# Kernel tuning notes

Measured on AMD Instinct MI355X. Metric: run time of the kernel, lower is better.

Reference implementation:

```python
import jax, jax.numpy as jnp
import numpy as np

N = 50000
T = 6
E = 800000
F_IN = 64
HID = 64
HEADS = 4
NEG_SLOPE = 0.2
BN_EPS = 1e-5


def _gat_layer(x, src, dst, W, att_src, att_dst, bias, concat):
    # x: [N, Fin]; W: [Fin, H*C]; att_*: [H, C]; src/dst: [E+N] (self loops appended)
    n = x.shape[0]
    H, C = att_src.shape
    xl = (x @ W).reshape(n, H, C)                     # [N, H, C]
    a_src = jnp.sum(xl * att_src[None], axis=-1)      # [N, H]
    a_dst = jnp.sum(xl * att_dst[None], axis=-1)      # [N, H]
    e = jax.nn.leaky_relu(a_src[src] + a_dst[dst], NEG_SLOPE)  # [E', H]
    # segment softmax over destination nodes (every node has a self loop)
    m = jax.ops.segment_max(e, dst, num_segments=n)
    ex = jnp.exp(e - m[dst])
    s = jax.ops.segment_sum(ex, dst, num_segments=n)
    alpha = ex / (s[dst] + 1e-16)                     # [E', H]
    msg = alpha[:, :, None] * xl[src]                 # [E', H, C]
    out = jax.ops.segment_sum(msg, dst, num_segments=n)  # [N, H, C]
    if concat:
        out = out.reshape(n, H * C)
    else:
        out = out.mean(axis=1)
    return out + bias


def _forward(x_seq, edge_index, W1, as1, ad1, b1, W2, as2, ad2, b2,
             cw1, cb1, g1, be1, cw2, cb2, g2, be2, lw1, lb1, lw2, lb2):
    n = x_seq.shape[1]
    self_loop = jnp.arange(n, dtype=edge_index.dtype)
    src = jnp.concatenate([edge_index[0], self_loop])
    dst = jnp.concatenate([edge_index[1], self_loop])

    def per_t(x):
        h = _gat_layer(x, src, dst, W1, as1, ad1, b1, concat=True)
        h = jax.nn.elu(h)
        h = _gat_layer(h, src, dst, W2, as2, ad2, b2, concat=False)
        h = jax.nn.elu(h)
        return h                                      # [N, HID]

    temporal = jax.vmap(per_t)(x_seq)                 # [T, N, HID]
    temporal = jnp.transpose(temporal, (1, 2, 0))     # [N, HID, T]

    def conv_bn_relu(t, cw, cb, g, be):
        y = jax.lax.conv_general_dilated(
            t, cw, window_strides=(1,), padding=[(1, 1)],
            dimension_numbers=('NCH', 'OIH', 'NCH')) + cb[None, :, None]
        # BatchNorm1d in eval mode, running_mean=0, running_var=1
        y = y * (g / jnp.sqrt(1.0 + BN_EPS))[None, :, None] + be[None, :, None]
        return jax.nn.relu(y)

    t = conv_bn_relu(temporal, cw1, cb1, g1, be1)
    t = conv_bn_relu(t, cw2, cb2, g2, be2)
    pooled = t.mean(axis=-1)                          # adaptive avg pool -> [N, HID]
    h = jax.nn.relu(pooled @ lw1 + lb1)
    logits = h @ lw2 + lb2                            # [N, 1]
    return logits


def setup_inputs() -> dict:
    key = jax.random.key(0)
    ks = jax.random.split(key, 20)
    C1 = HID // HEADS  # 16
    s = 0.1
    return {
        'x_seq': jax.random.normal(ks[0], (T, N, F_IN), jnp.float32),
        'edge_index': jax.random.randint(ks[1], (2, E), 0, N, jnp.int32),
        'W1': jax.random.normal(ks[2], (F_IN, HEADS * C1), jnp.float32) * s,
        'as1': jax.random.normal(ks[3], (HEADS, C1), jnp.float32) * s,
        'ad1': jax.random.normal(ks[4], (HEADS, C1), jnp.float32) * s,
        'b1': jnp.zeros((HEADS * C1,), jnp.float32),
        'W2': jax.random.normal(ks[5], (HID, HEADS * HID), jnp.float32) * s,
        'as2': jax.random.normal(ks[6], (HEADS, HID), jnp.float32) * s,
        'ad2': jax.random.normal(ks[7], (HEADS, HID), jnp.float32) * s,
        'b2': jnp.zeros((HID,), jnp.float32),
        'cw1': jax.random.normal(ks[8], (HID, HID, 3), jnp.float32) * s,
        'cb1': jnp.zeros((HID,), jnp.float32),
        'g1': jnp.ones((HID,), jnp.float32),
        'be1': jnp.zeros((HID,), jnp.float32),
        'cw2': jax.random.normal(ks[9], (HID, HID, 3), jnp.float32) * s,
        'cb2': jnp.zeros((HID,), jnp.float32),
        'g2': jnp.ones((HID,), jnp.float32),
        'be2': jnp.zeros((HID,), jnp.float32),
        'lw1': jax.random.normal(ks[10], (HID, HID // 2), jnp.float32) * s,
        'lb1': jnp.zeros((HID // 2,), jnp.float32),
        'lw2': jax.random.normal(ks[11], (HID // 2, 1), jnp.float32) * s,
        'lb2': jnp.zeros((1,), jnp.float32),
    }


def reference(x_seq, edge_index, W1, as1, ad1, b1, W2, as2, ad2, b2,
              cw1, cb1, g1, be1, cw2, cb2, g2, be2, lw1, lb1, lw2, lb2):
    return _forward(x_seq, edge_index, W1, as1, ad1, b1, W2, as2, ad2, b2,
                    cw1, cb1, g1, be1, cw2, cb2, g2, be2, lw1, lb1, lw2, lb2)
```

## Files before the change

kernel.cpp:

```cpp
#include <hip/hip_runtime.h>
#include <math.h>

#define NN 50000
#define EE 800000
#define TT 6

__device__ __forceinline__ float lrelu(float x){ return x > 0.f ? x : 0.2f*x; }
__device__ __forceinline__ float eluf(float x){ return x > 0.f ? x : expm1f(x); }

__global__ void k_init_counts(int* __restrict__ c){
  int i = blockIdx.x*256 + threadIdx.x;
  if (i < NN) c[i] = 1;
}

__global__ void k_hist(const int* __restrict__ dst, int* __restrict__ c){
  int i = blockIdx.x*256 + threadIdx.x;
  if (i < EE) atomicAdd(&c[dst[i]], 1);
}

__global__ void k_scanA(const int* __restrict__ cnt, int* __restrict__ excl,
                        int* __restrict__ bsum){
  __shared__ int sh[1024];
  int tid = threadIdx.x;
  int i = blockIdx.x*1024 + tid;
  int v = (i < NN) ? cnt[i] : 0;
  int x = v;
  sh[tid] = x; __syncthreads();
  for (int off = 1; off < 1024; off <<= 1){
    int y = (tid >= off) ? sh[tid - off] : 0;
    __syncthreads();
    x += y; sh[tid] = x; __syncthreads();
  }
  if (i < NN) excl[i] = x - v;
  if (tid == 1023) bsum[blockIdx.x] = x;
}

__global__ void k_scanB(int* __restrict__ bsum, int nb){
  if (threadIdx.x == 0){
    int run = 0;
    for (int b = 0; b < nb; ++b){ int t = bsum[b]; bsum[b] = run; run += t; }
  }
}

__global__ void k_scanC(const int* __restrict__ excl, const int* __restrict__ bsum,
                        int* __restrict__ rowptr, int* __restrict__ cursor){
  int i = blockIdx.x*1024 + threadIdx.x;
  if (i < NN){
    int v = excl[i] + bsum[blockIdx.x];
    rowptr[i] = v; cursor[i] = v;
  }
  if (i == 0) rowptr[NN] = EE + NN;
}

__global__ void k_scatter(const int* __restrict__ ei, int* __restrict__ cursor,
                          int* __restrict__ csr){
  int i = blockIdx.x*256 + threadIdx.x;
  if (i < EE){
    int d = ei[EE + i];
    int p = atomicAdd(&cursor[d], 1);
    csr[p] = ei[i];
  } else if (i < EE + NN){
    int v = i - EE;
    int p = atomicAdd(&cursor[v], 1);
    csr[p] = v;
  }
}

__global__ void k_prep(const float* __restrict__ W1, const float* __restrict__ as1,
                       const float* __restrict__ ad1,
                       const float* __restrict__ W2, const float* __restrict__ as2,
                       const float* __restrict__ ad2,
                       const float* __restrict__ cw1, const float* __restrict__ cw2,
                       const float* __restrict__ lw1,
                       float* __restrict__ Was1, float* __restrict__ Wad1,
                       float* __restrict__ Wat2, float* __restrict__ Wb,
                       float4* __restrict__ wq1, float4* __restrict__ wq2,
                       float* __restrict__ lw1t){
  int tid = threadIdx.x;
  int k = tid >> 2, h = tid & 3;
  float s1 = 0.f, d1 = 0.f, s2 = 0.f, d2 = 0.f;
  for (int c = 0; c < 16; ++c){
    float w = W1[k*64 + h*16 + c];
    s1 += w * as1[h*16 + c];
    d1 += w * ad1[h*16 + c];
  }
  for (int c = 0; c < 64; ++c){
    float w = W2[k*256 + h*64 + c];
    s2 += w * as2[h*64 + c];
    d2 += w * ad2[h*64 + c];
  }
  Was1[k*4+h] = s1; Wad1[k*4+h] = d1;
  Wat2[k*8 + h] = s2; Wat2[k*8 + 4 + h] = d2;
  for (int idx = tid; idx < 256*64; idx += 256){
    int kf = idx >> 6, c = idx & 63;
    int hh = kf >> 6, kk = kf & 63;
    Wb[idx] = W2[kk*256 + hh*64 + c];
  }
  for (int idx = tid; idx < 64*64; idx += 256){
    int o = idx >> 6, i = idx & 63;
    wq1[idx] = make_float4(cw1[o*192+i*3], cw1[o*192+i*3+1], cw1[o*192+i*3+2], 0.f);
    wq2[idx] = make_float4(cw2[o*192+i*3], cw2[o*192+i*3+1], cw2[o*192+i*3+2], 0.f);
  }
  for (int idx = tid; idx < 32*64; idx += 256){
    int j = idx >> 6, kk = idx & 63;
    lw1t[idx] = lw1[kk*32 + j];
  }
}

__global__ __launch_bounds__(256) void k_gemm_att1(const float* __restrict__ A,
                            const float* __restrict__ W,
                            const float* __restrict__ Was, const float* __restrict__ Wad,
                            float* __restrict__ Xl, float* __restrict__ a_src,
                            float* __restrict__ a_dst){
  __shared__ float At[64][16];
  int tid = threadIdx.x;
  int r0 = blockIdx.x * 16;
  {
    const float4* A4 = (const float4*)(A + (size_t)r0*64);
    float4 v = A4[tid];
    int r = tid >> 4, k4 = (tid & 15) << 2;
    At[k4+0][r] = v.x; At[k4+1][r] = v.y;
    At[k4+2][r] = v.z; At[k4+3][r] = v.w;
  }
  __syncthreads();
  int col = tid & 63;
  int rbase = (tid >> 6) << 2;
  float acc0=0.f, acc1=0.f, acc2=0.f, acc3=0.f;
  for (int k = 0; k < 64; ++k){
    float w = W[k*64 + col];
    float4 a4 = *(const float4*)&At[k][rbase];
    acc0 += a4.x*w; acc1 += a4.y*w; acc2 += a4.z*w; acc3 += a4.w*w;
  }
  Xl[(size_t)(r0+rbase+0)*64 + col] = acc0;
  Xl[(size_t)(r0+rbase+1)*64 + col] = acc1;
  Xl[(size_t)(r0+rbase+2)*64 + col] = acc2;
  Xl[(size_t)(r0+rbase+3)*64 + col] = acc3;
  if (tid < 128){
    int r = tid >> 3, jx = tid & 7;
    int h = jx & 3;
    const float* Wv = (jx < 4) ? Was : Wad;
    float a = 0.f;
    for (int k = 0; k < 64; ++k) a += At[k][r] * Wv[k*4 + h];
    if (jx < 4) a_src[(r0 + r)*4 + h] = a;
    else        a_dst[(r0 + r)*4 + h] = a;
  }
}

__global__ __launch_bounds__(256) void k_agg1(
                       const float* __restrict__ xl, const float* __restrict__ a_src,
                       const float* __restrict__ a_dst, const float* __restrict__ b1,
                       const float* __restrict__ Wat2,
                       const int* __restrict__ rowptr, const int* __restrict__ csr,
                       float* __restrict__ h1,
                       float* __restrict__ a_src2, float* __restrict__ a_dst2){
  int lane = threadIdx.x & 63;
  int wid  = threadIdx.x >> 6;
  int n = blockIdx.x*4 + wid;
  int h = lane >> 4;
  float ad = a_dst[n*4 + h];
  int rs = rowptr[n], re = rowptr[n+1];
  float s = 0.f, acc = 0.f;
  int j = rs;
  for (; j + 4 <= re; j += 4){
    int sn0=csr[j], sn1=csr[j+1], sn2=csr[j+2], sn3=csr[j+3];
    float e0=a_src[sn0*4+h], e1=a_src[sn1*4+h], e2=a_src[sn2*4+h], e3=a_src[sn3*4+h];
    float x0=xl[(size_t)sn0*64+lane], x1=xl[(size_t)sn1*64+lane];
    float x2=xl[(size_t)sn2*64+lane], x3=xl[(size_t)sn3*64+lane];
    float p0=__expf(lrelu(e0+ad)), p1=__expf(lrelu(e1+ad));
    float p2=__expf(lrelu(e2+ad)), p3=__expf(lrelu(e3+ad));
    s += p0; acc += p0*x0;
    s += p1; acc += p1*x1;
    s += p2; acc += p2*x2;
    s += p3; acc += p3*x3;
  }
  for (; j < re; ++j){
    int sn = csr[j];
    float p = __expf(lrelu(a_src[sn*4+h] + ad));
    float x = xl[(size_t)sn*64 + lane];
    s += p; acc += p*x;
  }
  float hv = eluf(acc/(s + 1e-16f) + b1[lane]);
  h1[(size_t)n*64 + lane] = hv;
  float4 wA = ((const float4*)Wat2)[lane*2];
  float4 wB = ((const float4*)Wat2)[lane*2 + 1];
  float p[8];
  p[0]=hv*wA.x; p[1]=hv*wA.y; p[2]=hv*wA.z; p[3]=hv*wA.w;
  p[4]=hv*wB.x; p[5]=hv*wB.y; p[6]=hv*wB.z; p[7]=hv*wB.w;
#pragma unroll
  for (int off = 32; off >= 1; off >>= 1){
#pragma unroll
    for (int q = 0; q < 8; ++q) p[q] += __shfl_xor(p[q], off);
  }
  if (lane == 0){
    ((float4*)a_src2)[n] = make_float4(p[0],p[1],p[2],p[3]);
    ((float4*)a_dst2)[n] = make_float4(p[4],p[5],p[6],p[7]);
  }
}

__global__ __launch_bounds__(256) void k_agg2(
                       const float* __restrict__ h1, const float* __restrict__ a_src,
                       const float* __restrict__ a_dst,
                       const int* __restrict__ rowptr, const int* __restrict__ csr,
                       float* __restrict__ agg){
  int lane = threadIdx.x & 63;
  int wid  = threadIdx.x >> 6;
  int n = blockIdx.x*4 + wid;
  float4 ad = ((const float4*)a_dst)[n];
  int rs = rowptr[n], re = rowptr[n+1];
  float s0=0.f,s1=0.f,s2=0.f,s3=0.f;
  float g0=0.f,g1=0.f,g2=0.f,g3=0.f;
  int j = rs;
  for (; j + 4 <= re; j += 4){
    int sa=csr[j], sb=csr[j+1], sc=csr[j+2], sd=csr[j+3];
    float4 ea = ((const float4*)a_src)[sa];
    float4 eb = ((const float4*)a_src)[sb];
    float4 ec = ((const float4*)a_src)[sc];
    float4 ed = ((const float4*)a_src)[sd];
    float xa = h1[(size_t)sa*64 + lane];
    float xb = h1[(size_t)sb*64 + lane];
    float xc = h1[(size_t)sc*64 + lane];
    float xd = h1[(size_t)sd*64 + lane];
    float pa0=__expf(lrelu(ea.x+ad.x)), pa1=__expf(lrelu(ea.y+ad.y));
    float pa2=__expf(lrelu(ea.z+ad.z)), pa3=__expf(lrelu(ea.w+ad.w));
    float pb0=__expf(lrelu(eb.x+ad.x)), pb1=__expf(lrelu(eb.y+ad.y));
    float pb2=__expf(lrelu(eb.z+ad.z)), pb3=__expf(lrelu(eb.w+ad.w));
    float pc0=__expf(lrelu(ec.x+ad.x)), pc1=__expf(lrelu(ec.y+ad.y));
    float pc2=__expf(lrelu(ec.z+ad.z)), pc3=__expf(lrelu(ec.w+ad.w));
    float pd0=__expf(lrelu(ed.x+ad.x)), pd1=__expf(lrelu(ed.y+ad.y));
    float pd2=__expf(lrelu(ed.z+ad.z)), pd3=__expf(lrelu(ed.w+ad.w));
    s0 += pa0+pb0+pc0+pd0; g0 += pa0*xa + pb0*xb + pc0*xc + pd0*xd;
    s1 += pa1+pb1+pc1+pd1; g1 += pa1*xa + pb1*xb + pc1*xc + pd1*xd;
    s2 += pa2+pb2+pc2+pd2; g2 += pa2*xa + pb2*xb + pc2*xc + pd2*xd;
    s3 += pa3+pb3+pc3+pd3; g3 += pa3*xa + pb3*xb + pc3*xc + pd3*xd;
  }
  for (; j < re; ++j){
    int sn = csr[j];
    float4 ev = ((const float4*)a_src)[sn];
    float x = h1[(size_t)sn*64 + lane];
    float p0=__expf(lrelu(ev.x+ad.x)), p1=__expf(lrelu(ev.y+ad.y));
    float p2=__expf(lrelu(ev.z+ad.z)), p3=__expf(lrelu(ev.w+ad.w));
    s0 += p0; g0 += p0*x;
    s1 += p1; g1 += p1*x;
    s2 += p2; g2 += p2*x;
    s3 += p3; g3 += p3*x;
  }
  size_t base = (size_t)n*256 + lane;
  agg[base      ] = g0/(s0 + 1e-16f);
  agg[base +  64] = g1/(s1 + 1e-16f);
  agg[base + 128] = g2/(s2 + 1e-16f);
  agg[base + 192] = g3/(s3 + 1e-16f);
}

__global__ __launch_bounds__(256) void k_out2(const float* __restrict__ agg,
                                              const float* __restrict__ Wb,
                                              const float* __restrict__ b2,
                                              float* __restrict__ ht){
  __shared__ float A[64*257];
  int tid = threadIdx.x;
  int lane = tid & 63;
  int w = __builtin_amdgcn_readfirstlane(tid >> 6);
  int r0 = blockIdx.x * 64;
  for (int jj = 0; jj < 64; ++jj){
    int m = jj*256 + tid;
    int row = m >> 8, k = m & 255;
    int rsrc = r0 + row; if (rsrc >= NN) rsrc = NN-1;
    A[row*257 + k] = agg[(size_t)rsrc*256 + k];
  }
  __syncthreads();
  const float* __restrict__ Wbw = Wb + w*16;
  float acc[16];
#pragma unroll
  for (int jq = 0; jq < 16; ++jq) acc[jq] = 0.f;
  const float* Ar = A + lane*257;
#pragma unroll 8
  for (int k = 0; k < 256; ++k){
    float a = Ar[k];
#pragma unroll
    for (int jq = 0; jq < 16; ++jq) acc[jq] += a * Wbw[(k<<6) + jq];
  }
  __syncthreads();
#pragma unroll
  for (int jq = 0; jq < 16; ++jq){
    int c = w*16 + jq;
    A[lane*65 + c] = eluf(0.25f*acc[jq] + b2[c]);
  }
  __syncthreads();
  for (int jj = 0; jj < 16; ++jj){
    int m = jj*256 + tid;
    int row = m >> 6, c = m & 63;
    int rdst = r0 + row;
    if (rdst < NN) ht[(size_t)rdst*64 + c] = A[row*65 + c];
  }
}

__global__ __launch_bounds__(256) void k_conv(const float* __restrict__ htb,
    const float4* __restrict__ wq1, const float* __restrict__ cb1,
    const float* __restrict__ g1,   const float* __restrict__ be1,
    const float4* __restrict__ wq2, const float* __restrict__ cb2,
    const float* __restrict__ g2,   const float* __restrict__ be2,
    float* __restrict__ pooledG){
  __shared__ float X[64*103];
  int tid  = threadIdx.x;
  int lane = tid & 63;
  int w    = __builtin_amdgcn_readfirstlane(tid >> 6);
  int nn   = lane & 15;
  int oq   = lane >> 4;
  int n0 = blockIdx.x*16;
  int n  = n0 + nn;
  int ob = w*16 + oq*4;

#pragma unroll
  for (int k = 0; k < 4; ++k){
    int p  = k*256 + tid;
    int ch = p & 63, ns = p >> 6;
    float xv[6];
#pragma unroll
    for (int t = 0; t < 6; ++t) xv[t] = htb[((size_t)t*NN + n0 + ns)*64 + ch];
#pragma unroll
    for (int t = 0; t < 6; ++t) X[ch*103 + t*17 + ns] = xv[t];
  }
  __syncthreads();

  float acc[4][6];
#pragma unroll
  for (int q = 0; q < 4; ++q){
    float c = cb1[ob+q];
#pragma unroll
    for (int t = 0; t < 6; ++t) acc[q][t] = c;
  }
  for (int i = 0; i < 64; ++i){
    const float* xp = X + i*103 + nn;
    float x1 = xp[0], x2 = xp[17], x3 = xp[34];
    float x4 = xp[51], x5 = xp[68], x6 = xp[85];
#pragma unroll
    for (int q = 0; q < 4; ++q){
      float4 wv = wq1[(ob+q)*64 + i];
      acc[q][0] += wv.y*x1 + wv.z*x2;
      acc[q][1] += wv.x*x1 + wv.y*x2 + wv.z*x3;
      acc[q][2] += wv.x*x2 + wv.y*x3 + wv.z*x4;
      acc[q][3] += wv.x*x3 + wv.y*x4 + wv.z*x5;
      acc[q][4] += wv.x*x4 + wv.y*x5 + wv.z*x6;
      acc[q][5] += wv.x*x5 + wv.y*x6;
    }
  }
  __syncthreads();
#pragma unroll
  for (int q = 0; q < 4; ++q){
    float bns = g1[ob+q]*rsqrtf(1.f + 1e-5f), be = be1[ob+q];
    float* xp = X + (ob+q)*103 + nn;
#pragma unroll
    for (int t = 0; t < 6; ++t) xp[t*17] = fmaxf(acc[q][t]*bns + be, 0.f);
  }
  __syncthreads();

#pragma unroll
  for (int q = 0; q < 4; ++q){
    float c = cb2[ob+q];
#pragma unroll
    for (int t = 0; t < 6; ++t) acc[q][t] = c;
  }
  for (int i = 0; i < 64; ++i){
    const float* xp = X + i*103 + nn;
    float x1 = xp[0], x2 = xp[17], x3 = xp[34];
    float x4 = xp[51], x5 = xp[68], x6 = xp[85];
#pragma unroll
    for (int q = 0; q < 4; ++q){
      float4 wv = wq2[(ob+q)*64 + i];
      acc[q][0] += wv.y*x1 + wv.z*x2;
      acc[q][1] += wv.x*x1 + wv.y*x2 + wv.z*x3;
      acc[q][2] += wv.x*x2 + wv.y*x3 + wv.z*x4;
      acc[q][3] += wv.x*x3 + wv.y*x4 + wv.z*x5;
      acc[q][4] += wv.x*x4 + wv.y*x5 + wv.z*x6;
      acc[q][5] += wv.x*x5 + wv.y*x6;
    }
  }
#pragma unroll
  for (int q = 0; q < 4; ++q){
    float bns = g2[ob+q]*rsqrtf(1.f + 1e-5f), be = be2[ob+q];
    float pooled = 0.f;
#pragma unroll
    for (int t = 0; t < 6; ++t) pooled += fmaxf(acc[q][t]*bns + be, 0.f);
    pooledG[(size_t)(ob+q)*NN + n] = pooled*(1.f/6.f);
  }
}

__global__ __launch_bounds__(256) void k_mlp(const float* __restrict__ pooledG,
    const float* __restrict__ lw1t, const float* __restrict__ lb1,
    const float* __restrict__ lw2,  const float* __restrict__ lb2,
    float* __restrict__ out){
  int lane = threadIdx.x & 63;
  int w = __builtin_amdgcn_readfirstlane(threadIdx.x >> 6);
  int n = (blockIdx.x*4 + w)*64 + lane;
  int nc = (n < NN) ? n : (NN-1);
  float p[64];
#pragma unroll 16
  for (int o = 0; o < 64; ++o) p[o] = pooledG[(size_t)o*NN + nc];
  float po = 0.f;
  for (int j = 0; j < 32; ++j){
    float hj = lb1[j];
#pragma unroll 16
    for (int k = 0; k < 64; ++k) hj += p[k] * lw1t[j*64 + k];
    po += fmaxf(hj, 0.f) * lw2[j];
  }
  if (n < NN) out[n] = po + lb2[0];
}

extern "C" void kernel_launch(void* const* d_in, const int* in_sizes, int n_in,
                              void* d_out, int out_size, void* d_ws, size_t ws_size,
                              hipStream_t stream) {
  const float* x_seq = (const float*)d_in[0];
  const int*   ei    = (const int*)  d_in[1];
  const float* W1  = (const float*)d_in[2];
  const float* as1 = (const float*)d_in[3];
  const float* ad1 = (const float*)d_in[4];
  const float* b1  = (const float*)d_in[5];
  const float* W2  = (const float*)d_in[6];
  const float* as2 = (const float*)d_in[7];
  const float* ad2 = (const float*)d_in[8];
  const float* b2  = (const float*)d_in[9];
  const float* cw1 = (const float*)d_in[10];
  const float* cb1 = (const float*)d_in[11];
  const float* g1  = (const float*)d_in[12];
  const float* be1 = (const float*)d_in[13];
  const float* cw2 = (const float*)d_in[14];
  const float* cb2 = (const float*)d_in[15];
  const float* g2  = (const float*)d_in[16];
  const float* be2 = (const float*)d_in[17];
  const float* lw1 = (const float*)d_in[18];
  const float* lb1 = (const float*)d_in[19];
  const float* lw2 = (const float*)d_in[20];
  const float* lb2 = (const float*)d_in[21];
  float* out = (float*)d_out;

  char* wp = (char*)d_ws;
  auto alloc = [&](size_t bytes) -> char* {
    char* p = wp; wp += (bytes + 255) & ~(size_t)255; return p;
  };
  int*   counts = (int*)  alloc(NN*sizeof(int));
  int*   excl   = (int*)  alloc(NN*sizeof(int));
  int*   bsum   = (int*)  alloc(64*sizeof(int));
  int*   rowptr = (int*)  alloc((NN+1)*sizeof(int));
  int*   cursor = (int*)  alloc(NN*sizeof(int));
  int*   csr    = (int*)  alloc((size_t)(EE+NN)*sizeof(int));
  float* a_src1 = (float*)alloc((size_t)NN*4*sizeof(float));
  float* a_dst1 = (float*)alloc((size_t)NN*4*sizeof(float));
  float* a_src2 = (float*)alloc((size_t)NN*4*sizeof(float));
  float* a_dst2 = (float*)alloc((size_t)NN*4*sizeof(float));
  float* h1     = (float*)alloc((size_t)NN*64*sizeof(float));
  float* agg    = (float*)alloc((size_t)NN*256*sizeof(float));
  float* xl1    = agg;
  float* htb    = (float*)alloc((size_t)TT*NN*64*sizeof(float));
  float* pooledG= (float*)alloc((size_t)64*NN*sizeof(float));
  float* Was1 = (float*)alloc(256*sizeof(float));
  float* Wad1 = (float*)alloc(256*sizeof(float));
  float* Wat2 = (float*)alloc(64*8*sizeof(float));
  float* Wb   = (float*)alloc(256*64*sizeof(float));
  float4* wq1 = (float4*)alloc(64*64*sizeof(float4));
  float4* wq2 = (float4*)alloc(64*64*sizeof(float4));
  float* lw1t = (float*)alloc(32*64*sizeof(float));

  const int NBSCAN = (NN + 1023)/1024;
  k_init_counts<<<(NN+255)/256, 256, 0, stream>>>(counts);
  k_hist<<<(EE+255)/256, 256, 0, stream>>>(ei + EE, counts);
  k_scanA<<<NBSCAN, 1024, 0, stream>>>(counts, excl, bsum);
  k_scanB<<<1, 64, 0, stream>>>(bsum, NBSCAN);
  k_scanC<<<NBSCAN, 1024, 0, stream>>>(excl, bsum, rowptr, cursor);
  k_scatter<<<(EE+NN+255)/256, 256, 0, stream>>>(ei, cursor, csr);
  k_prep<<<1, 256, 0, stream>>>(W1, as1, ad1, W2, as2, ad2, cw1, cw2, lw1,
                                Was1, Wad1, Wat2, Wb, wq1, wq2, lw1t);

  const int NOUT2 = (NN + 63)/64;
  for (int t = 0; t < TT; ++t){
    const float* xt = x_seq + (size_t)t*NN*64;
    k_gemm_att1<<<NN/16, 256, 0, stream>>>(xt, W1, Was1, Wad1, xl1, a_src1, a_dst1);
    k_agg1<<<NN/4, 256, 0, stream>>>(xl1, a_src1, a_dst1, b1, Wat2, rowptr, csr,
                                     h1, a_src2, a_dst2);
    k_agg2<<<NN/4, 256, 0, stream>>>(h1, a_src2, a_dst2, rowptr, csr, agg);
    k_out2<<<NOUT2, 256, 0, stream>>>(agg, Wb, b2, htb + (size_t)t*NN*64);
  }
  k_conv<<<NN/16, 256, 0, stream>>>(htb, wq1, cb1, g1, be1, wq2, cb2, g2, be2,
                                    pooledG);
  k_mlp<<<(NN+255)/256, 256, 0, stream>>>(pooledG, lw1t, lb1, lw2, lb2, out);
}
```

Before: 1.475 ms.

## Precompute edge attention weights in separate kernels and fuse conv with MLP head

After: 1.440 ms. 2.4% less time.

```diff
diff --git a/kernel.cpp b/kernel.cpp
--- a/kernel.cpp
+++ b/kernel.cpp
@@ -4,6 +4,7 @@
 #define NN 50000
 #define EE 800000
 #define TT 6
+#define SS (EE+NN)
 
 __device__ __forceinline__ float lrelu(float x){ return x > 0.f ? x : 0.2f*x; }
 __device__ __forceinline__ float eluf(float x){ return x > 0.f ? x : expm1f(x); }
@@ -49,20 +50,22 @@
     int v = excl[i] + bsum[blockIdx.x];
     rowptr[i] = v; cursor[i] = v;
   }
-  if (i == 0) rowptr[NN] = EE + NN;
+  if (i == 0) rowptr[NN] = SS;
 }
 
 __global__ void k_scatter(const int* __restrict__ ei, int* __restrict__ cursor,
-                          int* __restrict__ csr){
+                          int* __restrict__ csr, int* __restrict__ dstOf){
   int i = blockIdx.x*256 + threadIdx.x;
   if (i < EE){
     int d = ei[EE + i];
     int p = atomicAdd(&cursor[d], 1);
     csr[p] = ei[i];
-  } else if (i < EE + NN){
+    dstOf[p] = d;
+  } else if (i < SS){
     int v = i - EE;
     int p = atomicAdd(&cursor[v], 1);
     csr[p] = v;
+    dstOf[p] = v;
   }
 }
 
@@ -97,7 +100,7 @@
     Wb[idx] = W2[kk*256 + hh*64 + c];
   }
   for (int idx = tid; idx < 64*64; idx += 256){
-    int o = idx >> 6, i = idx & 63;
+    int i = idx >> 6, o = idx & 63;
     wq1[idx] = make_float4(cw1[o*192+i*3], cw1[o*192+i*3+1], cw1[o*192+i*3+2], 0.f);
     wq2[idx] = make_float4(cw2[o*192+i*3], cw2[o*192+i*3+1], cw2[o*192+i*3+2], 0.f);
   }
@@ -146,28 +149,53 @@
   }
 }
 
+__global__ __launch_bounds__(256) void k_edge1(const int* __restrict__ csr,
+                        const int* __restrict__ dstOf,
+                        const float* __restrict__ a_src, const float* __restrict__ a_dst,
+                        float* __restrict__ peh){
+  int k = blockIdx.x*256 + threadIdx.x;
+  if (k >= SS) return;
+  int sn = csr[k], dn = dstOf[k];
+  float4 as = ((const float4*)a_src)[sn];
+  float4 ad = ((const float4*)a_dst)[dn];
+  peh[k]                 = __expf(lrelu(as.x+ad.x));
+  peh[(size_t)SS + k]    = __expf(lrelu(as.y+ad.y));
+  peh[2*(size_t)SS + k]  = __expf(lrelu(as.z+ad.z));
+  peh[3*(size_t)SS + k]  = __expf(lrelu(as.w+ad.w));
+}
+
+__global__ __launch_bounds__(256) void k_edge2(const int* __restrict__ csr,
+                        const int* __restrict__ dstOf,
+                        const float* __restrict__ a_src, const float* __restrict__ a_dst,
+                        float4* __restrict__ pe4){
+  int k = blockIdx.x*256 + threadIdx.x;
+  if (k >= SS) return;
+  int sn = csr[k], dn = dstOf[k];
+  float4 as = ((const float4*)a_src)[sn];
+  float4 ad = ((const float4*)a_dst)[dn];
+  pe4[k] = make_float4(__expf(lrelu(as.x+ad.x)), __expf(lrelu(as.y+ad.y)),
+                       __expf(lrelu(as.z+ad.z)), __expf(lrelu(as.w+ad.w)));
+}
+
 __global__ __launch_bounds__(256) void k_agg1(
-                       const float* __restrict__ xl, const float* __restrict__ a_src,
-                       const float* __restrict__ a_dst, const float* __restrict__ b1,
-                       const float* __restrict__ Wat2,
+                       const float* __restrict__ xl, const float* __restrict__ peh,
+                       const float* __restrict__ b1, const float* __restrict__ Wat2,
                        const int* __restrict__ rowptr, const int* __restrict__ csr,
                        float* __restrict__ h1,
                        float* __restrict__ a_src2, float* __restrict__ a_dst2){
   int lane = threadIdx.x & 63;
-  int wid  = threadIdx.x >> 6;
+  int wid  = __builtin_amdgcn_readfirstlane(threadIdx.x >> 6);
   int n = blockIdx.x*4 + wid;
   int h = lane >> 4;
-  float ad = a_dst[n*4 + h];
+  const float* __restrict__ ph = peh + (size_t)h*SS;
   int rs = rowptr[n], re = rowptr[n+1];
   float s = 0.f, acc = 0.f;
   int j = rs;
   for (; j + 4 <= re; j += 4){
     int sn0=csr[j], sn1=csr[j+1], sn2=csr[j+2], sn3=csr[j+3];
-    float e0=a_src[sn0*4+h], e1=a_src[sn1*4+h], e2=a_src[sn2*4+h], e3=a_src[sn3*4+h];
+    float p0=ph[j], p1=ph[j+1], p2=ph[j+2], p3=ph[j+3];
     float x0=xl[(size_t)sn0*64+lane], x1=xl[(size_t)sn1*64+lane];
     float x2=xl[(size_t)sn2*64+lane], x3=xl[(size_t)sn3*64+lane];
-    float p0=__expf(lrelu(e0+ad)), p1=__expf(lrelu(e1+ad));
-    float p2=__expf(lrelu(e2+ad)), p3=__expf(lrelu(e3+ad));
     s += p0; acc += p0*x0;
     s += p1; acc += p1*x1;
     s += p2; acc += p2*x2;
@@ -175,7 +203,7 @@
   }
   for (; j < re; ++j){
     int sn = csr[j];
-    float p = __expf(lrelu(a_src[sn*4+h] + ad));
+    float p = ph[j];
     float x = xl[(size_t)sn*64 + lane];
     s += p; acc += p*x;
   }
@@ -198,51 +226,39 @@
 }
 
 __global__ __launch_bounds__(256) void k_agg2(
-                       const float* __restrict__ h1, const float* __restrict__ a_src,
-                       const float* __restrict__ a_dst,
+                       const float* __restrict__ h1, const float4* __restrict__ pe4,
                        const int* __restrict__ rowptr, const int* __restrict__ csr,
                        float* __restrict__ agg){
   int lane = threadIdx.x & 63;
-  int wid  = threadIdx.x >> 6;
+  int wid  = __builtin_amdgcn_readfirstlane(threadIdx.x >> 6);
   int n = blockIdx.x*4 + wid;
-  float4 ad = ((const float4*)a_dst)[n];
   int rs = rowptr[n], re = rowptr[n+1];
   float s0=0.f,s1=0.f,s2=0.f,s3=0.f;
   float g0=0.f,g1=0.f,g2=0.f,g3=0.f;
   int j = rs;
   for (; j + 4 <= re; j += 4){
     int sa=csr[j], sb=csr[j+1], sc=csr[j+2], sd=csr[j+3];
-    float4 ea = ((const float4*)a_src)[sa];
-    float4 eb = ((const float4*)a_src)[sb];
-    float4 ec = ((const float4*)a_src)[sc];
-    float4 ed = ((const float4*)a_src)[sd];
+    float4 pa = pe4[j];
+    float4 pb = pe4[j+1];
+    float4 pc = pe4[j+2];
+    float4 pd = pe4[j+3];
     float xa = h1[(size_t)sa*64 + lane];
     float xb = h1[(size_t)sb*64 + lane];
     float xc = h1[(size_t)sc*64 + lane];
     float xd = h1[(size_t)sd*64 + lane];
-    float pa0=__expf(lrelu(ea.x+ad.x)), pa1=__expf(lrelu(ea.y+ad.y));
-    float pa2=__expf(lrelu(ea.z+ad.z)), pa3=__expf(lrelu(ea.w+ad.w));
-    float pb0=__expf(lrelu(eb.x+ad.x)), pb1=__expf(lrelu(eb.y+ad.y));
-    float pb2=__expf(lrelu(eb.z+ad.z)), pb3=__expf(lrelu(eb.w+ad.w));
-    float pc0=__expf(lrelu(ec.x+ad.x)), pc1=__expf(lrelu(ec.y+ad.y));
-    float pc2=__expf(lrelu(ec.z+ad.z)), pc3=__expf(lrelu(ec.w+ad.w));
-    float pd0=__expf(lrelu(ed.x+ad.x)), pd1=__expf(lrelu(ed.y+ad.y));
-    float pd2=__expf(lrelu(ed.z+ad.z)), pd3=__expf(lrelu(ed.w+ad.w));
-    s0 += pa0+pb0+pc0+pd0; g0 += pa0*xa + pb0*xb + pc0*xc + pd0*xd;
-    s1 += pa1+pb1+pc1+pd1; g1 += pa1*xa + pb1*xb + pc1*xc + pd1*xd;
-    s2 += pa2+pb2+pc2+pd2; g2 += pa2*xa + pb2*xb + pc2*xc + pd2*xd;
-    s3 += pa3+pb3+pc3+pd3; g3 += pa3*xa + pb3*xb + pc3*xc + pd3*xd;
+    s0 += pa.x+pb.x+pc.x+pd.x; g0 += pa.x*xa + pb.x*xb + pc.x*xc + pd.x*xd;
+    s1 += pa.y+pb.y+pc.y+pd.y; g1 += pa.y*xa + pb.y*xb + pc.y*xc + pd.y*xd;
+    s2 += pa.z+pb.z+pc.z+pd.z; g2 += pa.z*xa + pb.z*xb + pc.z*xc + pd.z*xd;
+    s3 += pa.w+pb.w+pc.w+pd.w; g3 += pa.w*xa + pb.w*xb + pc.w*xc + pd.w*xd;
   }
   for (; j < re; ++j){
     int sn = csr[j];
-    float4 ev = ((const float4*)a_src)[sn];
+    float4 pv = pe4[j];
     float x = h1[(size_t)sn*64 + lane];
-    float p0=__expf(lrelu(ev.x+ad.x)), p1=__expf(lrelu(ev.y+ad.y));
-    float p2=__expf(lrelu(ev.z+ad.z)), p3=__expf(lrelu(ev.w+ad.w));
-    s0 += p0; g0 += p0*x;
-    s1 += p1; g1 += p1*x;
-    s2 += p2; g2 += p2*x;
-    s3 += p3; g3 += p3*x;
+    s0 += pv.x; g0 += pv.x*x;
+    s1 += pv.y; g1 += pv.y*x;
+    s2 += pv.z; g2 += pv.z*x;
+    s3 += pv.w; g3 += pv.w*x;
   }
   size_t base = (size_t)n*256 + lane;
   agg[base      ] = g0/(s0 + 1e-16f);
@@ -293,48 +309,52 @@
   }
 }
 
-__global__ __launch_bounds__(256) void k_conv(const float* __restrict__ htb,
+__global__ __launch_bounds__(512) void k_conv(const float* __restrict__ htb,
     const float4* __restrict__ wq1, const float* __restrict__ cb1,
     const float* __restrict__ g1,   const float* __restrict__ be1,
     const float4* __restrict__ wq2, const float* __restrict__ cb2,
     const float* __restrict__ g2,   const float* __restrict__ be2,
-    float* __restrict__ pooledG){
-  __shared__ float X[64*103];
+    const float* __restrict__ lw1t, const float* __restrict__ lb1,
+    const float* __restrict__ lw2,  const float* __restrict__ lb2,
+    float* __restrict__ out){
+  __shared__ float X[64*384];
+  __shared__ float pool_lds[64*64];
+  __shared__ float outp[8][64];
   int tid  = threadIdx.x;
   int lane = tid & 63;
   int w    = __builtin_amdgcn_readfirstlane(tid >> 6);
-  int nn   = lane & 15;
-  int oq   = lane >> 4;
-  int n0 = blockIdx.x*16;
-  int n  = n0 + nn;
-  int ob = w*16 + oq*4;
-
-#pragma unroll
-  for (int k = 0; k < 4; ++k){
-    int p  = k*256 + tid;
+  int n0 = blockIdx.x*64;
+  int n  = n0 + lane;
+  int ob = w*8;
+
+#pragma unroll
+  for (int it = 0; it < 8; ++it){
+    int p  = it*512 + tid;
     int ch = p & 63, ns = p >> 6;
+    int nsrc = n0 + ns; if (nsrc >= NN) nsrc = NN-1;
     float xv[6];
 #pragma unroll
-    for (int t = 0; t < 6; ++t) xv[t] = htb[((size_t)t*NN + n0 + ns)*64 + ch];
-#pragma unroll
-    for (int t = 0; t < 6; ++t) X[ch*103 + t*17 + ns] = xv[t];
-  }
-  __syncthreads();
-
-  float acc[4][6];
-#pragma unroll
-  for (int q = 0; q < 4; ++q){
+    for (int t = 0; t < 6; ++t) xv[t] = htb[((size_t)t*NN + nsrc)*64 + ch];
+#pragma unroll
+    for (int t = 0; t < 6; ++t) X[ch*384 + t*64 + ns] = xv[t];
+  }
+  __syncthreads();
+
+  float acc[8][6];
+#pragma unroll
+  for (int q = 0; q < 8; ++q){
     float c = cb1[ob+q];
 #pragma unroll
     for (int t = 0; t < 6; ++t) acc[q][t] = c;
   }
   for (int i = 0; i < 64; ++i){
-    const float* xp = X + i*103 + nn;
-    float x1 = xp[0], x2 = xp[17], x3 = xp[34];
-    float x4 = xp[51], x5 = xp[68], x6 = xp[85];
-#pragma unroll
-    for (int q = 0; q < 4; ++q){
-      float4 wv = wq1[(ob+q)*64 + i];
+    const float* xp = X + i*384 + lane;
+    float x1 = xp[0], x2 = xp[64], x3 = xp[128];
+    float x4 = xp[192], x5 = xp[256], x6 = xp[320];
+    const float4* wrow = wq1 + (i<<6) + ob;
+#pragma unroll
+    for (int q = 0; q < 8; ++q){
+      float4 wv = wrow[q];
       acc[q][0] += wv.y*x1 + wv.z*x2;
       acc[q][1] += wv.x*x1 + wv.y*x2 + wv.z*x3;
       acc[q][2] += wv.x*x2 + wv.y*x3 + wv.z*x4;
@@ -345,27 +365,28 @@
   }
   __syncthreads();
 #pragma unroll
-  for (int q = 0; q < 4; ++q){
+  for (int q = 0; q < 8; ++q){
     float bns = g1[ob+q]*rsqrtf(1.f + 1e-5f), be = be1[ob+q];
-    float* xp = X + (ob+q)*103 + nn;
-#pragma unroll
-    for (int t = 0; t < 6; ++t) xp[t*17] = fmaxf(acc[q][t]*bns + be, 0.f);
-  }
-  __syncthreads();
-
-#pragma unroll
-  for (int q = 0; q < 4; ++q){
+    float* xp = X + (ob+q)*384 + lane;
+#pragma unroll
+    for (int t = 0; t < 6; ++t) xp[t*64] = fmaxf(acc[q][t]*bns + be, 0.f);
+  }
+  __syncthreads();
+
+#pragma unroll
+  for (int q = 0; q < 8; ++q){
     float c = cb2[ob+q];
 #pragma unroll
     for (int t = 0; t < 6; ++t) acc[q][t] = c;
   }
   for (int i = 0; i < 64; ++i){
-    const float* xp = X + i*103 + nn;
-    float x1 = xp[0], x2 = xp[17], x3 = xp[34];
-    float x4 = xp[51], x5 = xp[68], x6 = xp[85];
-#pragma unroll
-    for (int q = 0; q < 4; ++q){
-      float4 wv = wq2[(ob+q)*64 + i];
+    const float* xp = X + i*384 + lane;
+    float x1 = xp[0], x2 = xp[64], x3 = xp[128];
+    float x4 = xp[192], x5 = xp[256], x6 = xp[320];
+    const float4* wrow = wq2 + (i<<6) + ob;
+#pragma unroll
+    for (int q = 0; q < 8; ++q){
+      float4 wv = wrow[q];
       acc[q][0] += wv.y*x1 + wv.z*x2;
       acc[q][1] += wv.x*x1 + wv.y*x2 + wv.z*x3;
       acc[q][2] += wv.x*x2 + wv.y*x3 + wv.z*x4;
@@ -375,34 +396,35 @@
     }
   }
 #pragma unroll
-  for (int q = 0; q < 4; ++q){
+  for (int q = 0; q < 8; ++q){
     float bns = g2[ob+q]*rsqrtf(1.f + 1e-5f), be = be2[ob+q];
     float pooled = 0.f;
 #pragma unroll
     for (int t = 0; t < 6; ++t) pooled += fmaxf(acc[q][t]*bns + be, 0.f);
-    pooledG[(size_t)(ob+q)*NN + n] = pooled*(1.f/6.f);
-  }
-}
-
-__global__ __launch_bounds__(256) void k_mlp(const float* __restrict__ pooledG,
-    const float* __restrict__ lw1t, const float* __restrict__ lb1,
-    const float* __restrict__ lw2,  const float* __restrict__ lb2,
-    float* __restrict__ out){
-  int lane = threadIdx.x & 63;
-  int w = __builtin_amdgcn_readfirstlane(threadIdx.x >> 6);
-  int n = (blockIdx.x*4 + w)*64 + lane;
-  int nc = (n < NN) ? n : (NN-1);
-  float p[64];
-#pragma unroll 16
-  for (int o = 0; o < 64; ++o) p[o] = pooledG[(size_t)o*NN + nc];
-  float po = 0.f;
-  for (int j = 0; j < 32; ++j){
-    float hj = lb1[j];
-#pragma unroll 16
-    for (int k = 0; k < 64; ++k) hj += p[k] * lw1t[j*64 + k];
-    po += fmaxf(hj, 0.f) * lw2[j];
-  }
-  if (n < NN) out[n] = po + lb2[0];
+    pool_lds[(ob+q)*64 + lane] = pooled*(1.f/6.f);
+  }
+  __syncthreads();
+
+  {
+    float po = 0.f;
+#pragma unroll
+    for (int jj = 0; jj < 4; ++jj){
+      int jdx = w*4 + jj;
+      float hj = lb1[jdx];
+      const float* lw = lw1t + jdx*64;
+#pragma unroll 8
+      for (int k = 0; k < 64; ++k) hj += pool_lds[k*64 + lane] * lw[k];
+      po += fmaxf(hj, 0.f) * lw2[jdx];
+    }
+    outp[w][lane] = po;
+  }
+  __syncthreads();
+  if (w == 0 && n < NN){
+    float r = lb2[0];
+#pragma unroll
+    for (int q = 0; q < 8; ++q) r += outp[q][lane];
+    out[n] = r;
+  }
 }
 
 extern "C" void kernel_launch(void* const* d_in, const int* in_sizes, int n_in,
@@ -441,7 +463,10 @@
   int*   bsum   = (int*)  alloc(64*sizeof(int));
   int*   rowptr = (int*)  alloc((NN+1)*sizeof(int));
   int*   cursor = (int*)  alloc(NN*sizeof(int));
-  int*   csr    = (int*)  alloc((size_t)(EE+NN)*sizeof(int));
+  int*   csr    = (int*)  alloc((size_t)SS*sizeof(int));
+  int*   dstOf  = (int*)  alloc((size_t)SS*sizeof(int));
+  float* peh    = (float*)alloc((size_t)4*SS*sizeof(float));
+  float4* pe4   = (float4*)alloc((size_t)SS*sizeof(float4));
   float* a_src1 = (float*)alloc((size_t)NN*4*sizeof(float));
   float* a_dst1 = (float*)alloc((size_t)NN*4*sizeof(float));
   float* a_src2 = (float*)alloc((size_t)NN*4*sizeof(float));
@@ -450,7 +475,6 @@
   float* agg    = (float*)alloc((size_t)NN*256*sizeof(float));
   float* xl1    = agg;
   float* htb    = (float*)alloc((size_t)TT*NN*64*sizeof(float));
-  float* pooledG= (float*)alloc((size_t)64*NN*sizeof(float));
   float* Was1 = (float*)alloc(256*sizeof(float));
   float* Wad1 = (float*)alloc(256*sizeof(float));
   float* Wat2 = (float*)alloc(64*8*sizeof(float));
@@ -465,20 +489,22 @@
   k_scanA<<<NBSCAN, 1024, 0, stream>>>(counts, excl, bsum);
   k_scanB<<<1, 64, 0, stream>>>(bsum, NBSCAN);
   k_scanC<<<NBSCAN, 1024, 0, stream>>>(excl, bsum, rowptr, cursor);
-  k_scatter<<<(EE+NN+255)/256, 256, 0, stream>>>(ei, cursor, csr);
+  k_scatter<<<(SS+255)/256, 256, 0, stream>>>(ei, cursor, csr, dstOf);
   k_prep<<<1, 256, 0, stream>>>(W1, as1, ad1, W2, as2, ad2, cw1, cw2, lw1,
                                 Was1, Wad1, Wat2, Wb, wq1, wq2, lw1t);
 
+  const int NEDGE = (SS + 255)/256;
   const int NOUT2 = (NN + 63)/64;
   for (int t = 0; t < TT; ++t){
     const float* xt = x_seq + (size_t)t*NN*64;
     k_gemm_att1<<<NN/16, 256, 0, stream>>>(xt, W1, Was1, Wad1, xl1, a_src1, a_dst1);
-    k_agg1<<<NN/4, 256, 0, stream>>>(xl1, a_src1, a_dst1, b1, Wat2, rowptr, csr,
+    k_edge1<<<NEDGE, 256, 0, stream>>>(csr, dstOf, a_src1, a_dst1, peh);
+    k_agg1<<<NN/4, 256, 0, stream>>>(xl1, peh, b1, Wat2, rowptr, csr,
                                      h1, a_src2, a_dst2);
-    k_agg2<<<NN/4, 256, 0, stream>>>(h1, a_src2, a_dst2, rowptr, csr, agg);
+    k_edge2<<<NEDGE, 256, 0, stream>>>(csr, dstOf, a_src2, a_dst2, pe4);
+    k_agg2<<<NN/4, 256, 0, stream>>>(h1, pe4, rowptr, csr, agg);
     k_out2<<<NOUT2, 256, 0, stream>>>(agg, Wb, b2, htb + (size_t)t*NN*64);
   }
-  k_conv<<<NN/16, 256, 0, stream>>>(htb, wq1, cb1, g1, be1, wq2, cb2, g2, be2,
-                                    pooledG);
-  k_mlp<<<(NN+255)/256, 256, 0, stream>>>(pooledG, lw1t, lb1, lw2, lb2, out);
-}
+  k_conv<<<(NN+63)/64, 512, 0, stream>>>(htb, wq1, cb1, g1, be1, wq2, cb2, g2, be2,
+                                         lw1t, lb1, lw2, lb2, out);
+}
```
